# Optimization experiments

Hardware: AMD Instinct MI355X
Metric: run time of the kernel (lower is better)

The kernel has to match this reference:

```python
import jax, jax.numpy as jnp
import numpy as np

N_HEAD = 16
N_EMBD = 1024
B, T = 4, 2048


def setup_inputs() -> dict:
    key = jax.random.key(0)
    ks = jax.random.split(key, 5)
    s_in = 1.0 / np.sqrt(N_EMBD)
    return {
        "x": jax.random.normal(ks[0], (B, T, N_EMBD), dtype=jnp.float32),
        "W_qkv": jax.random.normal(ks[1], (N_EMBD, 3 * N_EMBD), dtype=jnp.float32) * s_in,
        "b_qkv": jnp.zeros((3 * N_EMBD,), dtype=jnp.float32),
        "W_proj": jax.random.normal(ks[2], (N_EMBD, N_EMBD), dtype=jnp.float32) * s_in,
        "b_proj": jnp.zeros((N_EMBD,), dtype=jnp.float32),
    }


def reference(x, W_qkv, b_qkv, W_proj, b_proj):
    Bb, Tt, C = x.shape
    H = N_HEAD
    hd = C // H  # head dim
    qkv = x @ W_qkv + b_qkv                      # [B,T,3C]
    q, k, v = jnp.split(qkv, 3, axis=-1)
    # [B,H,T,hd]
    q = q.reshape(Bb, Tt, H, hd).transpose(0, 2, 1, 3)
    k = k.reshape(Bb, Tt, H, hd).transpose(0, 2, 1, 3)
    v = v.reshape(Bb, Tt, H, hd).transpose(0, 2, 1, 3)
    scale = 1.0 / np.sqrt(hd).astype(np.float32)
    att = jnp.einsum("bhqd,bhkd->bhqk", q, k) * scale
    causal = jnp.tril(jnp.ones((Tt, Tt), dtype=bool))
    att = jnp.where(causal, att, jnp.float32(-jnp.inf))
    att = jax.nn.softmax(att, axis=-1)
    y = jnp.einsum("bhqk,bhkd->bhqd", att, v)    # [B,H,T,hd]
    y = y.transpose(0, 2, 1, 3).reshape(Bb, Tt, C)
    return y @ W_proj + b_proj
```

## Files before the change

kernel.cpp:

```cpp
#include <hip/hip_runtime.h>
#include <hip/hip_bf16.h>
#include <math.h>

typedef unsigned short u16;
typedef _Float16 f16_t;
typedef f16_t f16x8 __attribute__((ext_vector_type(8)));
typedef float f32x4 __attribute__((ext_vector_type(4)));

#define N_HEADC 16
#define C_EMBD  1024
#define B_SZ    4
#define T_SEQ   2048
#define HD      64
#define M_TOT   (B_SZ * T_SEQ)

__device__ __forceinline__ u16 f2h(float f) {
    f16_t h = (f16_t)f;
    return __builtin_bit_cast(u16, h);
}
__device__ __forceinline__ unsigned pkf16(float a, float b) {
    unsigned lo = f2h(a), hi = f2h(b);
    return lo | (hi << 16);
}
__device__ __forceinline__ float fexp2(float x) {
#if __has_builtin(__builtin_amdgcn_exp2f)
    return __builtin_amdgcn_exp2f(x);
#else
    return exp2f(x);
#endif
}
__device__ __forceinline__ void gl_lds16(const u16* g, u16* l) {
    __builtin_amdgcn_global_load_lds(
        (const __attribute__((address_space(1))) unsigned int*)g,
        (__attribute__((address_space(3))) unsigned int*)l,
        16, 0, 0);
}

__global__ __launch_bounds__(256) void prep(const float* __restrict__ x,
                                            const float* __restrict__ Wqkv,
                                            const float* __restrict__ Wproj,
                                            u16* __restrict__ xh,
                                            u16* __restrict__ WqkvT,
                                            u16* __restrict__ WprojT) {
    __shared__ float tile[32][33];
    int bid = blockIdx.x, tid = threadIdx.x;
    if (bid < 8192) {
        int i = bid * 1024 + tid * 4;
        float4 v = *(const float4*)(x + i);
        ushort4 o;
        o.x = f2h(v.x); o.y = f2h(v.y); o.z = f2h(v.z); o.w = f2h(v.w);
        *(ushort4*)(xh + i) = o;
        return;
    }
    const float* in; u16* outp; int N, bx, by;
    if (bid < 8192 + 3072) {
        int b2 = bid - 8192; bx = b2 % 96; by = b2 / 96;
        in = Wqkv; outp = WqkvT; N = 3 * C_EMBD;
    } else {
        int b2 = bid - 11264; bx = b2 % 32; by = b2 / 32;
        in = Wproj; outp = WprojT; N = C_EMBD;
    }
    int tx = tid & 31, ty = tid >> 5;
    int n0 = bx * 32, k0 = by * 32;
    for (int i = ty; i < 32; i += 8)
        tile[i][tx] = in[(size_t)(k0 + i) * N + n0 + tx];
    __syncthreads();
    for (int i = ty; i < 32; i += 8)
        outp[(size_t)(n0 + i) * C_EMBD + k0 + tx] = f2h(tile[tx][i]);
}

__global__ __launch_bounds__(256) void gemm_qkv(const u16* __restrict__ A,
                                                const u16* __restrict__ BT,
                                                const float* __restrict__ bias,
                                                u16* __restrict__ qQ,
                                                u16* __restrict__ qK,
                                                u16* __restrict__ qVt) {
    const int NK = C_EMBD / 32;
    __shared__ __align__(16) u16 sS[2][2][128 * 32];
    int m0 = blockIdx.y * 128;
    int n0 = blockIdx.x * 128;
    int tid = threadIdx.x;
    int w = tid >> 6, lane = tid & 63;
    int m_off = (w & 1) * 64, n_off = (w >> 1) * 64;
    int quad = lane >> 4, rl = lane & 15;
    int srow = lane >> 2, sko = (lane & 3) * 8;

    f32x4 acc[4][4];
    #pragma unroll
    for (int i = 0; i < 4; ++i)
        #pragma unroll
        for (int j = 0; j < 4; ++j)
            acc[i][j] = f32x4{0.f, 0.f, 0.f, 0.f};

    const u16* gA0 = A + (size_t)(m0 + w * 32 + srow) * C_EMBD + sko;
    const u16* gA1 = gA0 + 16 * C_EMBD;
    const u16* gB0 = BT + (size_t)(n0 + w * 32 + srow) * C_EMBD + sko;
    const u16* gB1 = gB0 + 16 * C_EMBD;
    u16* lA[2] = { &sS[0][0][w * 32 * 32], &sS[1][0][w * 32 * 32] };
    u16* lB[2] = { &sS[0][1][w * 32 * 32], &sS[1][1][w * 32 * 32] };

    gl_lds16(gA0, lA[0]); gl_lds16(gA1, lA[0] + 512);
    gl_lds16(gB0, lB[0]); gl_lds16(gB1, lB[0] + 512);

    for (int kt = 0; kt < NK; ++kt) {
        __syncthreads();
        if (kt + 1 < NK) {
            gA0 += 32; gA1 += 32; gB0 += 32; gB1 += 32;
            int nb = (kt + 1) & 1;
            gl_lds16(gA0, lA[nb]); gl_lds16(gA1, lA[nb] + 512);
            gl_lds16(gB0, lB[nb]); gl_lds16(gB1, lB[nb] + 512);
        }
        const u16* pA = &sS[kt & 1][0][0];
        const u16* pB = &sS[kt & 1][1][0];
        f16x8 af[4], bfr[4];
        #pragma unroll
        for (int i = 0; i < 4; ++i)
            af[i] = *(const f16x8*)&pA[(m_off + i * 16 + rl) * 32 + quad * 8];
        #pragma unroll
        for (int j = 0; j < 4; ++j)
            bfr[j] = *(const f16x8*)&pB[(n_off + j * 16 + rl) * 32 + quad * 8];
        #pragma unroll
        for (int i = 0; i < 4; ++i)
            #pragma unroll
            for (int j = 0; j < 4; ++j)
                acc[i][j] = __builtin_amdgcn_mfma_f32_16x16x32_f16(af[i], bfr[j], acc[i][j], 0, 0, 0);
    }

    const float QSC = 0.18033688011112042f;
    int p = n0 >> 10;
    if (p < 2) {
        u16* dst = p == 0 ? qQ : qK;
        float sc = p == 0 ? QSC : 1.0f;
        #pragma unroll
        for (int j = 0; j < 4; ++j) {
            int n = n0 + n_off + j * 16 + rl;
            float bv = bias[n];
            int cch = n & 1023;
            int h = cch >> 6, d = cch & 63;
            #pragma unroll
            for (int i = 0; i < 4; ++i) {
                int mbase = m0 + m_off + i * 16 + quad * 4;
                int bb = mbase >> 11, t0 = mbase & 2047;
                size_t thbase = ((size_t)bb * N_HEADC + h) * T_SEQ;
                #pragma unroll
                for (int r = 0; r < 4; ++r)
                    dst[(thbase + t0 + r) * HD + d] = f2h((acc[i][j][r] + bv) * sc);
            }
        }
    } else {
        u16 (*tr)[136] = (u16 (*)[136])&sS[0][0][0];
        int bb = m0 >> 11, t0g = m0 & 2047;
        #pragma unroll
        for (int half = 0; half < 2; ++half) {
            __syncthreads();
            if (n_off == half * 64) {
                #pragma unroll
                for (int j = 0; j < 4; ++j) {
                    int rowr = j * 16 + rl;
                    float bv = bias[n0 + half * 64 + rowr];
                    #pragma unroll
                    for (int i = 0; i < 4; ++i) {
                        int mm = m_off + i * 16 + quad * 4;
                        *(unsigned*)&tr[rowr][mm]     = pkf16(acc[i][j][0] + bv, acc[i][j][1] + bv);
                        *(unsigned*)&tr[rowr][mm + 2] = pkf16(acc[i][j][2] + bv, acc[i][j][3] + bv);
                    }
                }
            }
            __syncthreads();
            #pragma unroll
            for (int s = 0; s < 4; ++s) {
                int task = s * 256 + tid;
                int nn = task >> 4, seg = task & 15;
                int n = (n0 & 1023) + half * 64 + nn;
                int h = n >> 6, d = n & 63;
                size_t di = (((size_t)bb * N_HEADC + h) * HD + d) * T_SEQ + t0g + seg * 8;
                *(uint4*)&qVt[di] = *(const uint4*)&tr[nn][seg * 8];
            }
        }
    }
}

__global__ __launch_bounds__(256) void gemm_proj(const u16* __restrict__ A,
                                                 const u16* __restrict__ BT,
                                                 const float* __restrict__ bias,
                                                 float* __restrict__ out) {
    const int NK = C_EMBD / 32;
    __shared__ __align__(16) u16 sS[2][2][128 * 32];
    int m0 = blockIdx.y * 128;
    int n0 = blockIdx.x * 128;
    int tid = threadIdx.x;
    int w = tid >> 6, lane = tid & 63;
    int m_off = (w & 1) * 64, n_off = (w >> 1) * 64;
    int quad = lane >> 4, rl = lane & 15;
    int srow = lane >> 2, sko = (lane & 3) * 8;

    f32x4 acc[4][4];
    #pragma unroll
    for (int i = 0; i < 4; ++i)
        #pragma unroll
        for (int j = 0; j < 4; ++j)
            acc[i][j] = f32x4{0.f, 0.f, 0.f, 0.f};

    const u16* gA0 = A + (size_t)(m0 + w * 32 + srow) * C_EMBD + sko;
    const u16* gA1 = gA0 + 16 * C_EMBD;
    const u16* gB0 = BT + (size_t)(n0 + w * 32 + srow) * C_EMBD + sko;
    const u16* gB1 = gB0 + 16 * C_EMBD;
    u16* lA[2] = { &sS[0][0][w * 32 * 32], &sS[1][0][w * 32 * 32] };
    u16* lB[2] = { &sS[0][1][w * 32 * 32], &sS[1][1][w * 32 * 32] };

    gl_lds16(gA0, lA[0]); gl_lds16(gA1, lA[0] + 512);
    gl_lds16(gB0, lB[0]); gl_lds16(gB1, lB[0] + 512);

    for (int kt = 0; kt < NK; ++kt) {
        __syncthreads();
        if (kt + 1 < NK) {
            gA0 += 32; gA1 += 32; gB0 += 32; gB1 += 32;
            int nb = (kt + 1) & 1;
            gl_lds16(gA0, lA[nb]); gl_lds16(gA1, lA[nb] + 512);
            gl_lds16(gB0, lB[nb]); gl_lds16(gB1, lB[nb] + 512);
        }
        const u16* pA = &sS[kt & 1][0][0];
        const u16* pB = &sS[kt & 1][1][0];
        f16x8 af[4], bfr[4];
        #pragma unroll
        for (int i = 0; i < 4; ++i)
            af[i] = *(const f16x8*)&pA[(m_off + i * 16 + rl) * 32 + quad * 8];
        #pragma unroll
        for (int j = 0; j < 4; ++j)
            bfr[j] = *(const f16x8*)&pB[(n_off + j * 16 + rl) * 32 + quad * 8];
        #pragma unroll
        for (int i = 0; i < 4; ++i)
            #pragma unroll
            for (int j = 0; j < 4; ++j)
                acc[i][j] = __builtin_amdgcn_mfma_f32_16x16x32_f16(af[i], bfr[j], acc[i][j], 0, 0, 0);
    }

    #pragma unroll
    for (int i = 0; i < 4; ++i) {
        int mbase = m0 + m_off + i * 16 + quad * 4;
        #pragma unroll
        for (int j = 0; j < 4; ++j) {
            int n = n0 + n_off + j * 16 + rl;
            float bv = bias[n];
            #pragma unroll
            for (int r = 0; r < 4; ++r)
                out[(size_t)(mbase + r) * C_EMBD + n] = acc[i][j][r] + bv;
        }
    }
}

__global__ __launch_bounds__(256) void attn_mfma(const u16* __restrict__ Qg,
                                                 const u16* __restrict__ Kg,
                                                 const u16* __restrict__ Vtg,
                                                 u16* __restrict__ yh) {
    int bx = blockIdx.x, h = blockIdx.y, b = blockIdx.z;
    const size_t hs = (size_t)T_SEQ * HD;
    const u16* Qp  = Qg  + ((size_t)b * N_HEADC + h) * hs;
    const u16* Kp  = Kg  + ((size_t)b * N_HEADC + h) * hs;
    const u16* Vtp = Vtg + ((size_t)b * N_HEADC + h) * hs;

    __shared__ __align__(16) u16 sK[2][2][64][32];
    __shared__ __align__(16) u16 sVt[2][2][64][32];
    __shared__ __align__(16) u16 sP[4][32][72];

    int tid = threadIdx.x;
    int lane = tid & 63, w = tid >> 6;
    int quad = lane >> 4, rl = lane & 15;
    u16* sPw = &sP[w][0][0];
    int srow = lane >> 2;
    int sch = (lane & 3) * 8;
    const f32x4 mneg = {-4.f, -4.f, -4.f, -4.f};

    const u16* gp0[4];
    u16* ld0[4]; u16* ld1[4];
    int gstep;
    if (w < 2) {
        gstep = 64 * HD;
        #pragma unroll
        for (int c = 0; c < 4; ++c) {
            gp0[c] = Kp + (size_t)(c * 16 + srow) * HD + w * 32 + sch;
            ld0[c] = &sK[0][w][c * 16][0];
            ld1[c] = &sK[1][w][c * 16][0];
        }
    } else {
        gstep = 64;
        #pragma unroll
        for (int c = 0; c < 4; ++c) {
            gp0[c] = Vtp + (size_t)(c * 16 + srow) * T_SEQ + (w - 2) * 32 + sch;
            ld0[c] = &sVt[0][w - 2][c * 16][0];
            ld1[c] = &sVt[1][w - 2][c * 16][0];
        }
    }

    #pragma unroll
    for (int phase = 0; phase < 2; ++phase) {
        int qt = phase == 0 ? (15 - bx) : bx;
        int q0w = qt * 128 + w * 32;
        int nkt = 2 * qt + 2;

        f16x8 qf[2][2];
        #pragma unroll
        for (int nt = 0; nt < 2; ++nt)
            #pragma unroll
            for (int ks = 0; ks < 2; ++ks)
                qf[nt][ks] = *(const f16x8*)&Qp[(size_t)(q0w + nt * 16 + rl) * HD + ks * 32 + quad * 8];

        f32x4 O[2][4];
        #pragma unroll
        for (int mi = 0; mi < 2; ++mi)
            #pragma unroll
            for (int nd = 0; nd < 4; ++nd)
                O[mi][nd] = f32x4{0.f, 0.f, 0.f, 0.f};
        float l_[2] = {0.f, 0.f};

        const u16* gp[4];
        #pragma unroll
        for (int c = 0; c < 4; ++c) gp[c] = gp0[c];

        __syncthreads();
        #pragma unroll
        for (int c = 0; c < 4; ++c) gl_lds16(gp[c], ld0[c]);

        for (int kt = 0; kt < nkt; ++kt) {
            __syncthreads();
            int buf = kt & 1;
            int k0 = kt * 64;
            if (kt + 1 < nkt) {
                u16* const* ldn = ((kt + 1) & 1) ? ld1 : ld0;
                #pragma unroll
                for (int c = 0; c < 4; ++c) {
                    gp[c] += gstep;
                    gl_lds16(gp[c], ldn[c]);
                }
            }
            if (k0 > q0w + 31) continue;

            f32x4 st[4][2];
            #pragma unroll
            for (int mt = 0; mt < 4; ++mt) {
                f16x8 ak0 = *(const f16x8*)&sK[buf][0][mt * 16 + rl][quad * 8];
                f16x8 ak1 = *(const f16x8*)&sK[buf][1][mt * 16 + rl][quad * 8];
                #pragma unroll
                for (int nt = 0; nt < 2; ++nt) {
                    f32x4 t = __builtin_amdgcn_mfma_f32_16x16x32_f16(ak0, qf[nt][0], mneg, 0, 0, 0);
                    st[mt][nt] = __builtin_amdgcn_mfma_f32_16x16x32_f16(ak1, qf[nt][1], t, 0, 0, 0);
                }
            }

            if (k0 + 63 > q0w) {
                #pragma unroll
                for (int mt = 0; mt < 4; ++mt)
                    #pragma unroll
                    for (int nt = 0; nt < 2; ++nt)
                        #pragma unroll
                        for (int r = 0; r < 4; ++r) {
                            int kpos = k0 + mt * 16 + quad * 4 + r;
                            int q = q0w + nt * 16 + rl;
                            if (kpos > q) st[mt][nt][r] = -INFINITY;
                        }
            }

            #pragma unroll
            for (int nt = 0; nt < 2; ++nt) {
                float lsum = 0.f;
                #pragma unroll
                for (int mt = 0; mt < 4; ++mt) {
                    float p0 = fexp2(st[mt][nt][0]);
                    float p1 = fexp2(st[mt][nt][1]);
                    float p2 = fexp2(st[mt][nt][2]);
                    float p3 = fexp2(st[mt][nt][3]);
                    lsum += (p0 + p1) + (p2 + p3);
                    *(uint2*)&sPw[(nt * 16 + rl) * 72 + mt * 16 + quad * 4] =
                        make_uint2(pkf16(p0, p1), pkf16(p2, p3));
                }
                l_[nt] += lsum;
            }

            #pragma unroll
            for (int ks = 0; ks < 2; ++ks) {
                f16x8 ap0 = *(const f16x8*)&sPw[(0 * 16 + rl) * 72 + ks * 32 + quad * 8];
                f16x8 ap1 = *(const f16x8*)&sPw[(1 * 16 + rl) * 72 + ks * 32 + quad * 8];
                #pragma unroll
                for (int nd = 0; nd < 4; ++nd) {
                    f16x8 bv = *(const f16x8*)&sVt[buf][ks][nd * 16 + rl][quad * 8];
                    O[0][nd] = __builtin_amdgcn_mfma_f32_16x16x32_f16(ap0, bv, O[0][nd], 0, 0, 0);
                    O[1][nd] = __builtin_amdgcn_mfma_f32_16x16x32_f16(ap1, bv, O[1][nd], 0, 0, 0);
                }
            }
        }

        #pragma unroll
        for (int nt = 0; nt < 2; ++nt) {
            l_[nt] += __shfl_xor(l_[nt], 16);
            l_[nt] += __shfl_xor(l_[nt], 32);
        }
        float linv[2] = {1.f / l_[0], 1.f / l_[1]};
        int idxq = quad * 4;
        #pragma unroll
        for (int mi = 0; mi < 2; ++mi)
            #pragma unroll
            for (int r = 0; r < 4; ++r) {
                float li = __shfl(linv[mi], idxq + r);
                int qg = q0w + mi * 16 + quad * 4 + r;
                size_t base = ((size_t)b * T_SEQ + qg) * C_EMBD + h * HD;
                #pragma unroll
                for (int nd = 0; nd < 4; ++nd)
                    yh[base + nd * 16 + rl] = f2h(O[mi][nd][r] * li);
            }
    }
}

extern "C" void kernel_launch(void* const* d_in, const int* in_sizes, int n_in,
                              void* d_out, int out_size, void* d_ws, size_t ws_size,
                              hipStream_t stream) {
    const float* x     = (const float*)d_in[0];
    const float* Wqkv  = (const float*)d_in[1];
    const float* bqkv  = (const float*)d_in[2];
    const float* Wproj = (const float*)d_in[3];
    const float* bproj = (const float*)d_in[4];
    float* out = (float*)d_out;

    char* ws = (char*)d_ws;
    u16* xh     = (u16*)(ws);
    u16* WqkvT  = (u16*)(ws + (size_t)16 * 1024 * 1024);
    u16* WprojT = (u16*)(ws + (size_t)22 * 1024 * 1024);
    u16* qQ     = (u16*)(ws + (size_t)24 * 1024 * 1024);
    u16* qK     = (u16*)(ws + (size_t)40 * 1024 * 1024);
    u16* qVt    = (u16*)(ws + (size_t)56 * 1024 * 1024);
    u16* yh     = (u16*)(ws + (size_t)72 * 1024 * 1024);

    prep<<<dim3(12288), dim3(256), 0, stream>>>(x, Wqkv, Wproj, xh, WqkvT, WprojT);
    gemm_qkv<<<dim3(3 * C_EMBD / 128, M_TOT / 128), dim3(256), 0, stream>>>(
        xh, WqkvT, bqkv, qQ, qK, qVt);
    attn_mfma<<<dim3(8, N_HEADC, B_SZ), dim3(256), 0, stream>>>(
        qQ, qK, qVt, yh);
    gemm_proj<<<dim3(C_EMBD / 128, M_TOT / 128), dim3(256), 0, stream>>>(
        yh, WprojT, bproj, out);
}
```

Baseline: 274.5 us.

## Enlarge GEMM tiles to 128x256 with 8 waves and triple-buffered LDS pipeline

Both the QKV and projection GEMMs move from 128x128 tiles with 4 waves and double buffering to 128x256 tiles with 8 waves. They now use a 3-stage LDS ring, explicit vmcnt waits with a raw s_barrier, and raised wave priority around the MFMA block. The aim is to hide global-to-LDS latency two stages ahead and to cut barrier stalls and per-tile B traffic. The cost is more LDS per block (72KB) and fewer blocks, which can lower occupancy. The V-transpose epilogue now loops over four 64-column chunks.

```diff
diff --git a/kernel.cpp b/kernel.cpp
--- a/kernel.cpp
+++ b/kernel.cpp
@@ -13,6 +13,13 @@
 #define T_SEQ   2048
 #define HD      64
 #define M_TOT   (B_SZ * T_SEQ)
+
+#define BM 128
+#define BN 256
+#define BK 32
+#define NT (C_EMBD / BK)
+#define A_T (BM * BK)
+#define B_T (BN * BK)
 
 __device__ __forceinline__ u16 f2h(float f) {
     f16_t h = (f16_t)f;
@@ -69,62 +76,77 @@
         outp[(size_t)(n0 + i) * C_EMBD + k0 + tx] = f2h(tile[tx][i]);
 }
 
-__global__ __launch_bounds__(256) void gemm_qkv(const u16* __restrict__ A,
+
+#define GEMM_PROLOGUE(Ap, BTp)                                                  \
+    int m0 = blockIdx.y * BM;                                                   \
+    int n0 = blockIdx.x * BN;                                                   \
+    int tid = threadIdx.x;                                                      \
+    int w = tid >> 6, lane = tid & 63;                                          \
+    int wm = w >> 2, wn = w & 3;                                                \
+    int quad = lane >> 4, rl = lane & 15;                                       \
+    int srow = lane >> 2, sko = (lane & 3) * 8;                                 \
+    f32x4 acc[4][4];                                                            \
+    _Pragma("unroll")                                                           \
+    for (int i = 0; i < 4; ++i)                                                 \
+        _Pragma("unroll")                                                       \
+        for (int j = 0; j < 4; ++j)                                             \
+            acc[i][j] = f32x4{0.f, 0.f, 0.f, 0.f};                              \
+    const u16* gA  = Ap  + (size_t)(m0 + w * 16 + srow) * C_EMBD + sko;         \
+    const u16* gB0 = BTp + (size_t)(n0 + w * 16 + srow) * C_EMBD + sko;         \
+    const u16* gB1 = gB0 + (size_t)128 * C_EMBD;                                \
+    u16* lA = sA + w * 512;                                                     \
+    u16* lB = sB + w * 512;                                                     \
+                                        \
+    gl_lds16(gA,      lA);                                                      \
+    gl_lds16(gB0,     lB);                                                      \
+    gl_lds16(gB1,     lB + 128 * BK);                                           \
+    gl_lds16(gA + BK,  lA + A_T);                                               \
+    gl_lds16(gB0 + BK, lB + B_T);                                               \
+    gl_lds16(gB1 + BK, lB + B_T + 128 * BK);                                    \
+    gA += 2 * BK; gB0 += 2 * BK; gB1 += 2 * BK;                                 \
+    int bufR = 0, bufS = 2;                                                     \
+    for (int t = 0; t < NT; ++t) {                                              \
+        if (t == NT - 1) asm volatile("s_waitcnt vmcnt(0)" ::: "memory");       \
+        else             asm volatile("s_waitcnt vmcnt(3)" ::: "memory");       \
+        asm volatile("s_barrier" ::: "memory");                                 \
+        const u16* pA = sA + bufR * A_T + (wm * 64) * BK;                       \
+        const u16* pB = sB + bufR * B_T + (wn * 64) * BK;                       \
+        f16x8 af[4], bfr[4];                                                    \
+        _Pragma("unroll")                                                       \
+        for (int i = 0; i < 4; ++i)                                             \
+            af[i] = *(const f16x8*)&pA[(i * 16 + rl) * BK + quad * 8];          \
+        _Pragma("unroll")                                                       \
+        for (int j = 0; j < 4; ++j)                                             \
+            bfr[j] = *(const f16x8*)&pB[(j * 16 + rl) * BK + quad * 8];         \
+        if (t + 2 < NT) {                                                       \
+            u16* dA = sA + bufS * A_T + w * 512;                                \
+            u16* dB = sB + bufS * B_T + w * 512;                                \
+            gl_lds16(gA,  dA);                                                  \
+            gl_lds16(gB0, dB);                                                  \
+            gl_lds16(gB1, dB + 128 * BK);                                       \
+            gA += BK; gB0 += BK; gB1 += BK;                                     \
+        }                                                                       \
+        __builtin_amdgcn_s_setprio(1);                                          \
+        _Pragma("unroll")                                                       \
+        for (int i = 0; i < 4; ++i)                                             \
+            _Pragma("unroll")                                                   \
+            for (int j = 0; j < 4; ++j)                                         \
+                acc[i][j] = __builtin_amdgcn_mfma_f32_16x16x32_f16(             \
+                    af[i], bfr[j], acc[i][j], 0, 0, 0);                         \
+        __builtin_amdgcn_s_setprio(0);                                          \
+        bufR = bufR == 2 ? 0 : bufR + 1;                                        \
+        bufS = bufS == 2 ? 0 : bufS + 1;                                        \
+    }
+
+__global__ __launch_bounds__(512) void gemm_qkv(const u16* __restrict__ A,
                                                 const u16* __restrict__ BT,
                                                 const float* __restrict__ bias,
                                                 u16* __restrict__ qQ,
                                                 u16* __restrict__ qK,
                                                 u16* __restrict__ qVt) {
-    const int NK = C_EMBD / 32;
-    __shared__ __align__(16) u16 sS[2][2][128 * 32];
-    int m0 = blockIdx.y * 128;
-    int n0 = blockIdx.x * 128;
-    int tid = threadIdx.x;
-    int w = tid >> 6, lane = tid & 63;
-    int m_off = (w & 1) * 64, n_off = (w >> 1) * 64;
-    int quad = lane >> 4, rl = lane & 15;
-    int srow = lane >> 2, sko = (lane & 3) * 8;
-
-    f32x4 acc[4][4];
-    #pragma unroll
-    for (int i = 0; i < 4; ++i)
-        #pragma unroll
-        for (int j = 0; j < 4; ++j)
-            acc[i][j] = f32x4{0.f, 0.f, 0.f, 0.f};
-
-    const u16* gA0 = A + (size_t)(m0 + w * 32 + srow) * C_EMBD + sko;
-    const u16* gA1 = gA0 + 16 * C_EMBD;
-    const u16* gB0 = BT + (size_t)(n0 + w * 32 + srow) * C_EMBD + sko;
-    const u16* gB1 = gB0 + 16 * C_EMBD;
-    u16* lA[2] = { &sS[0][0][w * 32 * 32], &sS[1][0][w * 32 * 32] };
-    u16* lB[2] = { &sS[0][1][w * 32 * 32], &sS[1][1][w * 32 * 32] };
-
-    gl_lds16(gA0, lA[0]); gl_lds16(gA1, lA[0] + 512);
-    gl_lds16(gB0, lB[0]); gl_lds16(gB1, lB[0] + 512);
-
-    for (int kt = 0; kt < NK; ++kt) {
-        __syncthreads();
-        if (kt + 1 < NK) {
-            gA0 += 32; gA1 += 32; gB0 += 32; gB1 += 32;
-            int nb = (kt + 1) & 1;
-            gl_lds16(gA0, lA[nb]); gl_lds16(gA1, lA[nb] + 512);
-            gl_lds16(gB0, lB[nb]); gl_lds16(gB1, lB[nb] + 512);
-        }
-        const u16* pA = &sS[kt & 1][0][0];
-        const u16* pB = &sS[kt & 1][1][0];
-        f16x8 af[4], bfr[4];
-        #pragma unroll
-        for (int i = 0; i < 4; ++i)
-            af[i] = *(const f16x8*)&pA[(m_off + i * 16 + rl) * 32 + quad * 8];
-        #pragma unroll
-        for (int j = 0; j < 4; ++j)
-            bfr[j] = *(const f16x8*)&pB[(n_off + j * 16 + rl) * 32 + quad * 8];
-        #pragma unroll
-        for (int i = 0; i < 4; ++i)
-            #pragma unroll
-            for (int j = 0; j < 4; ++j)
-                acc[i][j] = __builtin_amdgcn_mfma_f32_16x16x32_f16(af[i], bfr[j], acc[i][j], 0, 0, 0);
-    }
+    __shared__ __align__(16) u16 sA[3 * A_T];
+    __shared__ __align__(16) u16 sB[3 * B_T];
+    GEMM_PROLOGUE(A, BT)
 
     const float QSC = 0.18033688011112042f;
     int p = n0 >> 10;
@@ -133,13 +155,13 @@
         float sc = p == 0 ? QSC : 1.0f;
         #pragma unroll
         for (int j = 0; j < 4; ++j) {
-            int n = n0 + n_off + j * 16 + rl;
+            int n = n0 + wn * 64 + j * 16 + rl;
             float bv = bias[n];
             int cch = n & 1023;
             int h = cch >> 6, d = cch & 63;
             #pragma unroll
             for (int i = 0; i < 4; ++i) {
-                int mbase = m0 + m_off + i * 16 + quad * 4;
+                int mbase = m0 + wm * 64 + i * 16 + quad * 4;
                 int bb = mbase >> 11, t0 = mbase & 2047;
                 size_t thbase = ((size_t)bb * N_HEADC + h) * T_SEQ;
                 #pragma unroll
@@ -148,19 +170,19 @@
             }
         }
     } else {
-        u16 (*tr)[136] = (u16 (*)[136])&sS[0][0][0];
+        u16 (*tr)[136] = (u16 (*)[136])sA;
         int bb = m0 >> 11, t0g = m0 & 2047;
         #pragma unroll
-        for (int half = 0; half < 2; ++half) {
+        for (int c = 0; c < 4; ++c) {
             __syncthreads();
-            if (n_off == half * 64) {
+            if (wn == c) {
                 #pragma unroll
                 for (int j = 0; j < 4; ++j) {
                     int rowr = j * 16 + rl;
-                    float bv = bias[n0 + half * 64 + rowr];
+                    float bv = bias[n0 + c * 64 + rowr];
                     #pragma unroll
                     for (int i = 0; i < 4; ++i) {
-                        int mm = m_off + i * 16 + quad * 4;
+                        int mm = wm * 64 + i * 16 + quad * 4;
                         *(unsigned*)&tr[rowr][mm]     = pkf16(acc[i][j][0] + bv, acc[i][j][1] + bv);
                         *(unsigned*)&tr[rowr][mm + 2] = pkf16(acc[i][j][2] + bv, acc[i][j][3] + bv);
                     }
@@ -168,11 +190,11 @@
             }
             __syncthreads();
             #pragma unroll
-            for (int s = 0; s < 4; ++s) {
-                int task = s * 256 + tid;
+            for (int s = 0; s < 2; ++s) {
+                int task = s * 512 + tid;
                 int nn = task >> 4, seg = task & 15;
-                int n = (n0 & 1023) + half * 64 + nn;
-                int h = n >> 6, d = n & 63;
+                int ch = (n0 & 1023) + c * 64 + nn;
+                int h = ch >> 6, d = ch & 63;
                 size_t di = (((size_t)bb * N_HEADC + h) * HD + d) * T_SEQ + t0g + seg * 8;
                 *(uint4*)&qVt[di] = *(const uint4*)&tr[nn][seg * 8];
             }
@@ -180,67 +202,20 @@
     }
 }
 
-__global__ __launch_bounds__(256) void gemm_proj(const u16* __restrict__ A,
+__global__ __launch_bounds__(512) void gemm_proj(const u16* __restrict__ A,
                                                  const u16* __restrict__ BT,
                                                  const float* __restrict__ bias,
                                                  float* __restrict__ out) {
-    const int NK = C_EMBD / 32;
-    __shared__ __align__(16) u16 sS[2][2][128 * 32];
-    int m0 = blockIdx.y * 128;
-    int n0 = blockIdx.x * 128;
-    int tid = threadIdx.x;
-    int w = tid >> 6, lane = tid & 63;
-    int m_off = (w & 1) * 64, n_off = (w >> 1) * 64;
-    int quad = lane >> 4, rl = lane & 15;
-    int srow = lane >> 2, sko = (lane & 3) * 8;
-
-    f32x4 acc[4][4];
-    #pragma unroll
-    for (int i = 0; i < 4; ++i)
-        #pragma unroll
-        for (int j = 0; j < 4; ++j)
-            acc[i][j] = f32x4{0.f, 0.f, 0.f, 0.f};
-
-    const u16* gA0 = A + (size_t)(m0 + w * 32 + srow) * C_EMBD + sko;
-    const u16* gA1 = gA0 + 16 * C_EMBD;
-    const u16* gB0 = BT + (size_t)(n0 + w * 32 + srow) * C_EMBD + sko;
-    const u16* gB1 = gB0 + 16 * C_EMBD;
-    u16* lA[2] = { &sS[0][0][w * 32 * 32], &sS[1][0][w * 32 * 32] };
-    u16* lB[2] = { &sS[0][1][w * 32 * 32], &sS[1][1][w * 32 * 32] };
-
-    gl_lds16(gA0, lA[0]); gl_lds16(gA1, lA[0] + 512);
-    gl_lds16(gB0, lB[0]); gl_lds16(gB1, lB[0] + 512);
-
-    for (int kt = 0; kt < NK; ++kt) {
-        __syncthreads();
-        if (kt + 1 < NK) {
-            gA0 += 32; gA1 += 32; gB0 += 32; gB1 += 32;
-            int nb = (kt + 1) & 1;
-            gl_lds16(gA0, lA[nb]); gl_lds16(gA1, lA[nb] + 512);
-            gl_lds16(gB0, lB[nb]); gl_lds16(gB1, lB[nb] + 512);
-        }
-        const u16* pA = &sS[kt & 1][0][0];
-        const u16* pB = &sS[kt & 1][1][0];
-        f16x8 af[4], bfr[4];
-        #pragma unroll
-        for (int i = 0; i < 4; ++i)
-            af[i] = *(const f16x8*)&pA[(m_off + i * 16 + rl) * 32 + quad * 8];
-        #pragma unroll
-        for (int j = 0; j < 4; ++j)
-            bfr[j] = *(const f16x8*)&pB[(n_off + j * 16 + rl) * 32 + quad * 8];
-        #pragma unroll
-        for (int i = 0; i < 4; ++i)
-            #pragma unroll
-            for (int j = 0; j < 4; ++j)
-                acc[i][j] = __builtin_amdgcn_mfma_f32_16x16x32_f16(af[i], bfr[j], acc[i][j], 0, 0, 0);
-    }
+    __shared__ __align__(16) u16 sA[3 * A_T];
+    __shared__ __align__(16) u16 sB[3 * B_T];
+    GEMM_PROLOGUE(A, BT)
 
     #pragma unroll
     for (int i = 0; i < 4; ++i) {
-        int mbase = m0 + m_off + i * 16 + quad * 4;
+        int mbase = m0 + wm * 64 + i * 16 + quad * 4;
         #pragma unroll
         for (int j = 0; j < 4; ++j) {
-            int n = n0 + n_off + j * 16 + rl;
+            int n = n0 + wn * 64 + j * 16 + rl;
             float bv = bias[n];
             #pragma unroll
             for (int r = 0; r < 4; ++r)
@@ -430,10 +405,10 @@
     u16* yh     = (u16*)(ws + (size_t)72 * 1024 * 1024);
 
     prep<<<dim3(12288), dim3(256), 0, stream>>>(x, Wqkv, Wproj, xh, WqkvT, WprojT);
-    gemm_qkv<<<dim3(3 * C_EMBD / 128, M_TOT / 128), dim3(256), 0, stream>>>(
+    gemm_qkv<<<dim3(3 * C_EMBD / BN, M_TOT / BM), dim3(512), 0, stream>>>(
         xh, WqkvT, bqkv, qQ, qK, qVt);
     attn_mfma<<<dim3(8, N_HEADC, B_SZ), dim3(256), 0, stream>>>(
         qQ, qK, qVt, yh);
-    gemm_proj<<<dim3(C_EMBD / 128, M_TOT / 128), dim3(256), 0, stream>>>(
+    gemm_proj<<<dim3(C_EMBD / BN, M_TOT / BM), dim3(512), 0, stream>>>(
         yh, WprojT, bproj, out);
 }
```

Measured after the change: 251.7 us. -8.3%, faster.
